# Kernel tuning notes

Hardware: AMD Instinct MI355X
Metric: run time of the kernel (lower is better)

## Reference

```python
import jax, jax.numpy as jnp
import numpy as np

B, L, D = 8, 4096, 768
EPS = 1e-5


def layer_norm(x, g, b):
    mu = jnp.mean(x, axis=-1, keepdims=True)
    var = jnp.mean(jnp.square(x - mu), axis=-1, keepdims=True)
    return (x - mu) * jax.lax.rsqrt(var + EPS) * g + b


def conv1d_same(x_blc, w_oik, b_o):
    # x_blc: [B, L, C] -> torch Conv1d(C, C, 3, padding=1) on [B, C, L]
    x_ncw = jnp.swapaxes(x_blc, 1, 2)
    y = jax.lax.conv_general_dilated(
        x_ncw, w_oik, window_strides=(1,), padding=[(1, 1)],
        dimension_numbers=("NCW", "OIW", "NCW"))
    y = y + b_o[None, :, None]
    return jnp.swapaxes(y, 1, 2)


def simple_ssm(u, a_p, b_p, c_p, d_p):
    # Diagonal SSM: h_t = sigmoid(a)*h_{t-1} + b*u_t ; y_t = c*h_t + d*u_t
    a = jax.nn.sigmoid(a_p)  # [D]

    def step(h, ut):  # h, ut: [B, D]
        h = a * h + b_p * ut
        return h, c_p * h

    h0 = jnp.zeros((u.shape[0], u.shape[2]), u.dtype)
    _, y = jax.lax.scan(step, h0, jnp.swapaxes(u, 0, 1))  # y: [L, B, D]
    return jnp.swapaxes(y, 0, 1) + d_p * u


def setup_inputs() -> dict:
    key = jax.random.key(0)
    ks = jax.random.split(key, 16)
    s_lin = 1.0 / np.sqrt(D)
    s_conv = 1.0 / np.sqrt(3 * D)
    return {
        "x": jax.random.normal(ks[0], (B, L, D), jnp.float32),
        "ln_g": jnp.ones((D,), jnp.float32),
        "ln_b": jnp.zeros((D,), jnp.float32),
        "Wi": jax.random.normal(ks[1], (D, 2 * D), jnp.float32) * s_lin,
        "bi": jnp.zeros((2 * D,), jnp.float32),
        "Wf_conv": jax.random.normal(ks[2], (D, D, 3), jnp.float32) * s_conv,
        "bf_conv": jnp.zeros((D,), jnp.float32),
        "af": jax.random.normal(ks[3], (D,), jnp.float32),
        "bf": jax.random.normal(ks[4], (D,), jnp.float32) * 0.5,
        "cf": jax.random.normal(ks[5], (D,), jnp.float32) * 0.5,
        "df": jax.random.normal(ks[6], (D,), jnp.float32) * 0.5,
        "Wb_conv": jax.random.normal(ks[7], (D, D, 3), jnp.float32) * s_conv,
        "bb_conv": jnp.zeros((D,), jnp.float32),
        "ab": jax.random.normal(ks[8], (D,), jnp.float32),
        "bb": jax.random.normal(ks[9], (D,), jnp.float32) * 0.5,
        "cb": jax.random.normal(ks[10], (D,), jnp.float32) * 0.5,
        "db": jax.random.normal(ks[11], (D,), jnp.float32) * 0.5,
        "Wo": jax.random.normal(ks[12], (D, D), jnp.float32) * s_lin,
        "bo": jnp.zeros((D,), jnp.float32),
    }


def reference(x, ln_g, ln_b, Wi, bi, Wf_conv, bf_conv, af, bf, cf, df,
              Wb_conv, bb_conv, ab, bb, cb, db, Wo, bo):
    residual = x
    xn = layer_norm(x, ln_g, ln_b)
    proj = xn @ Wi + bi                      # [B, L, 2D]
    xg, z = proj[..., :D], proj[..., D:]
    # forward branch
    f = conv1d_same(xg, Wf_conv, bf_conv)
    f = simple_ssm(f, af, bf, cf, df)
    # backward branch (flip along sequence)
    b_in = jnp.flip(xg, axis=1)
    bb_out = conv1d_same(b_in, Wb_conv, bb_conv)
    bb_out = simple_ssm(bb_out, ab, bb, cb, db)
    bb_out = jnp.flip(bb_out, axis=1)
    zg = jax.nn.silu(z)
    y = f * zg + bb_out * zg
    return y @ Wo + bo + residual
```

## Files before the change

kernel.cpp:

```cpp
#include <hip/hip_runtime.h>
#include <cstdint>
#include <cstddef>
#include <math.h>

#define L_SEQ 4096
#define D_DIM 768
#define B_SZ 8
#define M_ROWS (B_SZ * L_SEQ)
#define CHUNK 64

typedef __bf16 bf16x8 __attribute__((ext_vector_type(8)));
typedef float floatx4 __attribute__((ext_vector_type(4)));

__global__ __launch_bounds__(256) void ln_kernel(const float* __restrict__ x,
                                                 const float* __restrict__ g,
                                                 const float* __restrict__ b,
                                                 __bf16* __restrict__ xn) {
  __shared__ float red[256];
  const int tid = threadIdx.x;
  const size_t row = blockIdx.x;
  const float* xr = x + row * D_DIM;
  float v0 = xr[tid];
  float v1 = xr[tid + 256];
  float v2 = xr[tid + 512];
  red[tid] = v0 + v1 + v2;
  __syncthreads();
  for (int off = 128; off > 0; off >>= 1) {
    if (tid < off) red[tid] += red[tid + off];
    __syncthreads();
  }
  float mu = red[0] * (1.0f / D_DIM);
  __syncthreads();
  float d0 = v0 - mu, d1 = v1 - mu, d2 = v2 - mu;
  red[tid] = d0 * d0 + d1 * d1 + d2 * d2;
  __syncthreads();
  for (int off = 128; off > 0; off >>= 1) {
    if (tid < off) red[tid] += red[tid + off];
    __syncthreads();
  }
  float rs = rsqrtf(red[0] * (1.0f / D_DIM) + 1e-5f);
  __bf16* xo = xn + row * D_DIM;
  xo[tid]       = (__bf16)(d0 * rs * g[tid]       + b[tid]);
  xo[tid + 256] = (__bf16)(d1 * rs * g[tid + 256] + b[tid + 256]);
  xo[tid + 512] = (__bf16)(d2 * rs * g[tid + 512] + b[tid + 512]);
}

template<int MODE>
__global__ __launch_bounds__(256) void gemm_kernel(
    const __bf16* __restrict__ A,
    const __bf16* __restrict__ Bt,
    const float* __restrict__ bias,
    const float* __restrict__ resid,
    __bf16* __restrict__ out0,
    __bf16* __restrict__ out1,
    float* __restrict__ outf,
    int K) {
  __shared__ __bf16 As[128 * 40];
  __shared__ __bf16 Bs[128 * 40];
  const int tid  = threadIdx.x;
  const int tileM = blockIdx.x;
  const int tileN = blockIdx.y;
  const int lane = tid & 63;
  const int wv   = tid >> 6;
  const int wm   = wv >> 1;
  const int wn   = wv & 1;
  const int l15  = lane & 15;
  const int quad = lane >> 4;
  const int sr = tid >> 2;
  const int sc = (tid & 3) * 8;

  floatx4 acc[4][4];
#pragma unroll
  for (int i = 0; i < 4; ++i)
#pragma unroll
    for (int j = 0; j < 4; ++j)
#pragma unroll
      for (int r = 0; r < 4; ++r) acc[i][j][r] = 0.0f;

  for (int kt = 0; kt < K; kt += 32) {
    __syncthreads();
#pragma unroll
    for (int p = 0; p < 2; ++p) {
      int r = sr + p * 64;
      bf16x8 av;
      if (MODE == 1 || MODE == 2) {
        int grow = tileM * 128 + r;
        int bidx = grow >> 12;
        int l    = grow & (L_SEQ - 1);
        int kblk = kt / D_DIM;
        int i0   = kt - kblk * D_DIM;
        int lsrc = (MODE == 1) ? (l + kblk - 1) : (L_SEQ - l - kblk);
        if (lsrc >= 0 && lsrc < L_SEQ) {
          av = *(const bf16x8*)(A + ((size_t)(bidx * L_SEQ + lsrc)) * D_DIM + i0 + sc);
        } else {
#pragma unroll
          for (int q = 0; q < 8; ++q) av[q] = (__bf16)0.0f;
        }
      } else {
        size_t grow = (size_t)(tileM * 128 + r);
        av = *(const bf16x8*)(A + grow * (size_t)K + kt + sc);
      }
      *(bf16x8*)(&As[r * 40 + sc]) = av;
      size_t gn = (size_t)(tileN * 128 + r);
      bf16x8 bv = *(const bf16x8*)(Bt + gn * (size_t)K + kt + sc);
      *(bf16x8*)(&Bs[r * 40 + sc]) = bv;
    }
    __syncthreads();

    bf16x8 afr[4], bfr[4];
#pragma unroll
    for (int i = 0; i < 4; ++i)
      afr[i] = *(const bf16x8*)(&As[(wm * 64 + i * 16 + l15) * 40 + quad * 8]);
#pragma unroll
    for (int j = 0; j < 4; ++j)
      bfr[j] = *(const bf16x8*)(&Bs[(wn * 64 + j * 16 + l15) * 40 + quad * 8]);
#pragma unroll
    for (int i = 0; i < 4; ++i)
#pragma unroll
      for (int j = 0; j < 4; ++j)
        acc[i][j] = __builtin_amdgcn_mfma_f32_16x16x32_bf16(afr[i], bfr[j], acc[i][j], 0, 0, 0);
  }

#pragma unroll
  for (int i = 0; i < 4; ++i) {
#pragma unroll
    for (int j = 0; j < 4; ++j) {
#pragma unroll
      for (int r = 0; r < 4; ++r) {
        int row = tileM * 128 + wm * 64 + i * 16 + quad * 4 + r;
        int col = tileN * 128 + wn * 64 + j * 16 + l15;
        float v = acc[i][j][r] + bias[col];
        if (MODE == 0) {
          if (col < D_DIM) {
            out0[(size_t)row * D_DIM + col] = (__bf16)v;
          } else {
            float s = v / (1.0f + expf(-v));
            out1[(size_t)row * D_DIM + (col - D_DIM)] = (__bf16)s;
          }
        } else if (MODE == 3) {
          size_t o = (size_t)row * D_DIM + col;
          outf[o] = v + resid[o];
        } else {
          out0[(size_t)row * D_DIM + col] = (__bf16)v;
        }
      }
    }
  }
}


__global__ __launch_bounds__(256) void scan1_kernel(
    const float* __restrict__ ap0, const float* __restrict__ bp0,
    const float* __restrict__ ap1, const float* __restrict__ bp1,
    const __bf16* __restrict__ u0, const __bf16* __restrict__ u1,
    float* __restrict__ hl) {
  int idx = blockIdx.x * 256 + threadIdx.x;
  int d = idx % D_DIM;
  int rest = idx / D_DIM;
  int chunk = rest & 63;
  int tb = rest >> 6;
  int b = tb & 7;
  int tensor = tb >> 3;
  const float* ap = tensor ? ap1 : ap0;
  const float* bp = tensor ? bp1 : bp0;
  const __bf16* u = (tensor ? u1 : u0) +
      ((size_t)(b * L_SEQ + chunk * CHUNK)) * D_DIM + d;
  float a  = 1.0f / (1.0f + expf(-ap[d]));
  float bb = bp[d];
  float h = 0.0f;
  for (int t = 0; t < CHUNK; ++t) {
    h = a * h + bb * (float)u[(size_t)t * D_DIM];
  }
  hl[(size_t)idx] = h;
}

__global__ __launch_bounds__(256) void scan2_kernel(
    const float* __restrict__ ap0, const float* __restrict__ ap1,
    float* __restrict__ hl) {
  int idx = blockIdx.x * 256 + threadIdx.x;
  int d = idx % D_DIM;
  int tb = idx / D_DIM;
  int tensor = tb >> 3;
  const float* ap = tensor ? ap1 : ap0;
  float a = 1.0f / (1.0f + expf(-ap[d]));
  float aT = a * a;
  aT = aT * aT;
  aT = aT * aT;
  aT = aT * aT;
  aT = aT * aT;
  aT = aT * aT;
  float* base = hl + (size_t)tb * 64 * D_DIM + d;
  float carry = 0.0f;
  for (int c = 0; c < 64; ++c) {
    float* p = base + (size_t)c * D_DIM;
    float tmp = *p;
    *p = carry;
    carry = aT * carry + tmp;
  }
}

__global__ __launch_bounds__(256) void scan3_kernel(
    const float* __restrict__ ap0, const float* __restrict__ bp0,
    const float* __restrict__ cp0, const float* __restrict__ dp0,
    const float* __restrict__ ap1, const float* __restrict__ bp1,
    const float* __restrict__ cp1, const float* __restrict__ dp1,
    __bf16* __restrict__ u0, __bf16* __restrict__ u1,
    const float* __restrict__ hl) {
  int idx = blockIdx.x * 256 + threadIdx.x;
  int d = idx % D_DIM;
  int rest = idx / D_DIM;
  int chunk = rest & 63;
  int tb = rest >> 6;
  int b = tb & 7;
  int tensor = tb >> 3;
  const float* ap = tensor ? ap1 : ap0;
  const float* bp = tensor ? bp1 : bp0;
  const float* cp = tensor ? cp1 : cp0;
  const float* dp = tensor ? dp1 : dp0;
  __bf16* u = (tensor ? u1 : u0) +
      ((size_t)(b * L_SEQ + chunk * CHUNK)) * D_DIM + d;
  float a  = 1.0f / (1.0f + expf(-ap[d]));
  float bb = bp[d];
  float cc = cp[d];
  float dd = dp[d];
  float h = hl[(size_t)idx];
  for (int t = 0; t < CHUNK; ++t) {
    float uv = (float)u[(size_t)t * D_DIM];
    h = a * h + bb * uv;
    u[(size_t)t * D_DIM] = (__bf16)(cc * h + dd * uv);
  }
}

__global__ __launch_bounds__(256) void gate_kernel(const __bf16* __restrict__ f,
                                                   const __bf16* __restrict__ bbuf,
                                                   const __bf16* __restrict__ zg,
                                                   __bf16* __restrict__ y) {
  size_t idx = (size_t)blockIdx.x * 256 + threadIdx.x;
  int d = (int)(idx % D_DIM);
  size_t rl = idx / D_DIM;
  int l = (int)(rl & (L_SEQ - 1));
  size_t b = rl >> 12;
  size_t src = ((b << 12) + (size_t)(L_SEQ - 1 - l)) * D_DIM + d;
  float v = ((float)f[idx] + (float)bbuf[src]) * (float)zg[idx];
  y[idx] = (__bf16)v;
}

__global__ __launch_bounds__(256) void tr_kernel(const float* __restrict__ in,
                                                 __bf16* __restrict__ out,
                                                 int Kdim, int Ndim) {
  int idx = blockIdx.x * 256 + threadIdx.x;
  if (idx >= Kdim * Ndim) return;
  int n = idx / Kdim;
  int k = idx - n * Kdim;
  out[idx] = (__bf16)in[(size_t)k * Ndim + n];
}

__global__ __launch_bounds__(256) void trconv_kernel(const float* __restrict__ in,
                                                     __bf16* __restrict__ out) {
  int idx = blockIdx.x * 256 + threadIdx.x;
  if (idx >= D_DIM * 2304) return;
  int o = idx / 2304;
  int rem = idx - o * 2304;
  int k = rem / D_DIM;
  int i = rem - k * D_DIM;
  out[idx] = (__bf16)in[(size_t)o * 2304 + i * 3 + k];
}

extern "C" void kernel_launch(void* const* d_in, const int* in_sizes, int n_in,
                              void* d_out, int out_size, void* d_ws, size_t ws_size,
                              hipStream_t stream) {
  const float* x    = (const float*)d_in[0];
  const float* ln_g = (const float*)d_in[1];
  const float* ln_b = (const float*)d_in[2];
  const float* Wi   = (const float*)d_in[3];
  const float* bi   = (const float*)d_in[4];
  const float* Wf   = (const float*)d_in[5];
  const float* bfc  = (const float*)d_in[6];
  const float* af   = (const float*)d_in[7];
  const float* bfp  = (const float*)d_in[8];
  const float* cfp  = (const float*)d_in[9];
  const float* dfp  = (const float*)d_in[10];
  const float* Wb   = (const float*)d_in[11];
  const float* bbc  = (const float*)d_in[12];
  const float* ab   = (const float*)d_in[13];
  const float* bbp  = (const float*)d_in[14];
  const float* cbp  = (const float*)d_in[15];
  const float* dbp  = (const float*)d_in[16];
  const float* Wo   = (const float*)d_in[17];
  const float* bo   = (const float*)d_in[18];
  float* out = (float*)d_out;

  char* ws = (char*)d_ws;
  const size_t BLD = (size_t)B_SZ * L_SEQ * D_DIM;
  __bf16* ws0 = (__bf16*)(ws);
  __bf16* ws1 = (__bf16*)(ws + BLD * 2);
  __bf16* ws2 = (__bf16*)(ws + BLD * 4);
  __bf16* ws3 = (__bf16*)(ws + BLD * 6);
  __bf16* wit = (__bf16*)(ws + BLD * 8);
  __bf16* wft = wit + (size_t)1536 * 768;
  __bf16* wbt = wft + (size_t)768 * 2304;
  __bf16* wot = wbt + (size_t)768 * 2304;
  float* hl = (float*)(ws + BLD * 2);
  const size_t needed = BLD * 8 +
      ((size_t)1536 * 768 + 2 * (size_t)768 * 2304 + (size_t)768 * 768) * 2;
  if (ws_size < needed) return;

  tr_kernel<<<(768 * 1536 + 255) / 256, 256, 0, stream>>>(Wi, wit, 768, 1536);
  trconv_kernel<<<(768 * 2304 + 255) / 256, 256, 0, stream>>>(Wf, wft);
  trconv_kernel<<<(768 * 2304 + 255) / 256, 256, 0, stream>>>(Wb, wbt);
  tr_kernel<<<(768 * 768 + 255) / 256, 256, 0, stream>>>(Wo, wot, 768, 768);

  ln_kernel<<<M_ROWS, 256, 0, stream>>>(x, ln_g, ln_b, ws0);

  gemm_kernel<0><<<dim3(M_ROWS / 128, 1536 / 128), 256, 0, stream>>>(
      ws0, wit, bi, nullptr, ws1, ws2, nullptr, 768);

  gemm_kernel<1><<<dim3(M_ROWS / 128, 768 / 128), 256, 0, stream>>>(
      ws1, wft, bfc, nullptr, ws0, nullptr, nullptr, 2304);
  gemm_kernel<2><<<dim3(M_ROWS / 128, 768 / 128), 256, 0, stream>>>(
      ws1, wbt, bbc, nullptr, ws3, nullptr, nullptr, 2304);

  {
    const int n1 = 2 * B_SZ * 64 * D_DIM;
    scan1_kernel<<<n1 / 256, 256, 0, stream>>>(af, bfp, ab, bbp, ws0, ws3, hl);
    const int n2 = 2 * B_SZ * D_DIM;
    scan2_kernel<<<n2 / 256, 256, 0, stream>>>(af, ab, hl);
    scan3_kernel<<<n1 / 256, 256, 0, stream>>>(af, bfp, cfp, dfp,
                                               ab, bbp, cbp, dbp,
                                               ws0, ws3, hl);
  }

  gate_kernel<<<(unsigned)(BLD / 256), 256, 0, stream>>>(ws0, ws3, ws2, ws1);

  gemm_kernel<3><<<dim3(M_ROWS / 128, 768 / 128), 256, 0, stream>>>(
      ws1, wot, bo, x, nullptr, nullptr, out, 768);
}
```

Baseline: 901.7 us.

## Use direct global-to-LDS loads in GEMM and swap grid axes for reuse

The GEMM tile loads now use global_load_lds (buffer-to-LDS DMA), so data no longer passes through registers. Conv boundary rows point at a small zeroed buffer instead of taking a branch. The LDS row stride drops from 40 to 32 because the DMA writes contiguously, which may bring back LDS bank conflicts on fragment reads. The grid is also transposed so N-tiles vary fastest, letting neighbouring blocks share the same A rows in cache, and the k-block/offset bookkeeping becomes incremental instead of a division.

Result: faster. 880.5 us (-2.3%).

```diff
diff --git a/kernel.cpp b/kernel.cpp
--- a/kernel.cpp
+++ b/kernel.cpp
@@ -11,6 +11,9 @@
 
 typedef __bf16 bf16x8 __attribute__((ext_vector_type(8)));
 typedef float floatx4 __attribute__((ext_vector_type(4)));
+
+#define GLP(p)  ((__attribute__((address_space(1))) const void*)(const void*)(p))
+#define LDSP(p) ((__attribute__((address_space(3))) void*)(void*)(p))
 
 __global__ __launch_bounds__(256) void ln_kernel(const float* __restrict__ x,
                                                  const float* __restrict__ g,
@@ -54,20 +57,45 @@
     __bf16* __restrict__ out0,
     __bf16* __restrict__ out1,
     float* __restrict__ outf,
+    const __bf16* __restrict__ zbuf,
     int K) {
-  __shared__ __bf16 As[128 * 40];
-  __shared__ __bf16 Bs[128 * 40];
-  const int tid  = threadIdx.x;
-  const int tileM = blockIdx.x;
-  const int tileN = blockIdx.y;
+  __shared__ __bf16 As[128 * 32];
+  __shared__ __bf16 Bs[128 * 32];
+  const int tid   = threadIdx.x;
+  const int tileN = blockIdx.x;
+  const int tileM = blockIdx.y;
   const int lane = tid & 63;
-  const int wv   = tid >> 6;
-  const int wm   = wv >> 1;
-  const int wn   = wv & 1;
+  const int w    = tid >> 6;
+  const int wm   = w >> 1;
+  const int wn   = w & 1;
   const int l15  = lane & 15;
   const int quad = lane >> 4;
-  const int sr = tid >> 2;
-  const int sc = (tid & 3) * 8;
+  const int colg = (lane & 3) * 8;
+  const int rsub = lane >> 2;
+
+  const int rowA0 = w * 32 + rsub;
+  const int rowA1 = rowA0 + 16;
+
+  const __bf16* gB0 = Bt + (size_t)(tileN * 128 + rowA0) * K + colg;
+  const __bf16* gB1 = Bt + (size_t)(tileN * 128 + rowA1) * K + colg;
+
+  const __bf16* gA0 = nullptr;
+  const __bf16* gA1 = nullptr;
+  int bl0 = 0, bl1 = 0, l0 = 0, l1 = 0;
+  if (MODE == 1 || MODE == 2) {
+    int gr0 = tileM * 128 + rowA0;
+    int gr1 = tileM * 128 + rowA1;
+    bl0 = gr0 >> 12; l0 = gr0 & (L_SEQ - 1);
+    bl1 = gr1 >> 12; l1 = gr1 & (L_SEQ - 1);
+  } else {
+    gA0 = A + (size_t)(tileM * 128 + rowA0) * K + colg;
+    gA1 = A + (size_t)(tileM * 128 + rowA1) * K + colg;
+  }
+
+  __bf16* ldsA0 = &As[(w * 32) * 32];
+  __bf16* ldsA1 = &As[(w * 32 + 16) * 32];
+  __bf16* ldsB0 = &Bs[(w * 32) * 32];
+  __bf16* ldsB1 = &Bs[(w * 32 + 16) * 32];
 
   floatx4 acc[4][4];
 #pragma unroll
@@ -77,48 +105,43 @@
 #pragma unroll
       for (int r = 0; r < 4; ++r) acc[i][j][r] = 0.0f;
 
+  int kblk = 0, i0 = 0;
   for (int kt = 0; kt < K; kt += 32) {
     __syncthreads();
-#pragma unroll
-    for (int p = 0; p < 2; ++p) {
-      int r = sr + p * 64;
-      bf16x8 av;
-      if (MODE == 1 || MODE == 2) {
-        int grow = tileM * 128 + r;
-        int bidx = grow >> 12;
-        int l    = grow & (L_SEQ - 1);
-        int kblk = kt / D_DIM;
-        int i0   = kt - kblk * D_DIM;
-        int lsrc = (MODE == 1) ? (l + kblk - 1) : (L_SEQ - l - kblk);
-        if (lsrc >= 0 && lsrc < L_SEQ) {
-          av = *(const bf16x8*)(A + ((size_t)(bidx * L_SEQ + lsrc)) * D_DIM + i0 + sc);
-        } else {
-#pragma unroll
-          for (int q = 0; q < 8; ++q) av[q] = (__bf16)0.0f;
-        }
-      } else {
-        size_t grow = (size_t)(tileM * 128 + r);
-        av = *(const bf16x8*)(A + grow * (size_t)K + kt + sc);
-      }
-      *(bf16x8*)(&As[r * 40 + sc]) = av;
-      size_t gn = (size_t)(tileN * 128 + r);
-      bf16x8 bv = *(const bf16x8*)(Bt + gn * (size_t)K + kt + sc);
-      *(bf16x8*)(&Bs[r * 40 + sc]) = bv;
+    const __bf16* pa0;
+    const __bf16* pa1;
+    if (MODE == 1 || MODE == 2) {
+      int ls0 = (MODE == 1) ? (l0 + kblk - 1) : (L_SEQ - l0 - kblk);
+      int ls1 = (MODE == 1) ? (l1 + kblk - 1) : (L_SEQ - l1 - kblk);
+      pa0 = (ls0 >= 0 && ls0 < L_SEQ)
+          ? A + ((size_t)(bl0 << 12) + (size_t)ls0) * D_DIM + i0 + colg : zbuf;
+      pa1 = (ls1 >= 0 && ls1 < L_SEQ)
+          ? A + ((size_t)(bl1 << 12) + (size_t)ls1) * D_DIM + i0 + colg : zbuf;
+    } else {
+      pa0 = gA0 + kt;
+      pa1 = gA1 + kt;
     }
+    __builtin_amdgcn_global_load_lds(GLP(pa0), LDSP(ldsA0), 16, 0, 0);
+    __builtin_amdgcn_global_load_lds(GLP(pa1), LDSP(ldsA1), 16, 0, 0);
+    __builtin_amdgcn_global_load_lds(GLP(gB0 + kt), LDSP(ldsB0), 16, 0, 0);
+    __builtin_amdgcn_global_load_lds(GLP(gB1 + kt), LDSP(ldsB1), 16, 0, 0);
     __syncthreads();
 
     bf16x8 afr[4], bfr[4];
 #pragma unroll
     for (int i = 0; i < 4; ++i)
-      afr[i] = *(const bf16x8*)(&As[(wm * 64 + i * 16 + l15) * 40 + quad * 8]);
+      afr[i] = *(const bf16x8*)(&As[(wm * 64 + i * 16 + l15) * 32 + quad * 8]);
 #pragma unroll
     for (int j = 0; j < 4; ++j)
-      bfr[j] = *(const bf16x8*)(&Bs[(wn * 64 + j * 16 + l15) * 40 + quad * 8]);
+      bfr[j] = *(const bf16x8*)(&Bs[(wn * 64 + j * 16 + l15) * 32 + quad * 8]);
 #pragma unroll
     for (int i = 0; i < 4; ++i)
 #pragma unroll
       for (int j = 0; j < 4; ++j)
         acc[i][j] = __builtin_amdgcn_mfma_f32_16x16x32_bf16(afr[i], bfr[j], acc[i][j], 0, 0, 0);
+
+    i0 += 32;
+    if (i0 == D_DIM) { i0 = 0; ++kblk; }
   }
 
 #pragma unroll
@@ -148,7 +171,6 @@
   }
 }
 
-
 __global__ __launch_bounds__(256) void scan1_kernel(
     const float* __restrict__ ap0, const float* __restrict__ bp0,
     const float* __restrict__ ap1, const float* __restrict__ bp1,
@@ -183,12 +205,8 @@
   int tensor = tb >> 3;
   const float* ap = tensor ? ap1 : ap0;
   float a = 1.0f / (1.0f + expf(-ap[d]));
-  float aT = a * a;
-  aT = aT * aT;
-  aT = aT * aT;
-  aT = aT * aT;
-  aT = aT * aT;
-  aT = aT * aT;
+  float aT = a * a;  aT = aT * aT;  aT = aT * aT;
+  aT = aT * aT;      aT = aT * aT;  aT = aT * aT;
   float* base = hl + (size_t)tb * 64 * D_DIM + d;
   float carry = 0.0f;
   for (int c = 0; c < 64; ++c) {
@@ -265,6 +283,8 @@
   int i = rem - k * D_DIM;
   out[idx] = (__bf16)in[(size_t)o * 2304 + i * 3 + k];
 }
+
+__global__ void zero_kernel(__bf16* z) { z[threadIdx.x] = (__bf16)0.0f; }
 
 extern "C" void kernel_launch(void* const* d_in, const int* in_sizes, int n_in,
                               void* d_out, int out_size, void* d_ws, size_t ws_size,
@@ -300,11 +320,13 @@
   __bf16* wft = wit + (size_t)1536 * 768;
   __bf16* wbt = wft + (size_t)768 * 2304;
   __bf16* wot = wbt + (size_t)768 * 2304;
+  __bf16* zbuf = wot + (size_t)768 * 768;
   float* hl = (float*)(ws + BLD * 2);
   const size_t needed = BLD * 8 +
-      ((size_t)1536 * 768 + 2 * (size_t)768 * 2304 + (size_t)768 * 768) * 2;
+      ((size_t)1536 * 768 + 2 * (size_t)768 * 2304 + (size_t)768 * 768) * 2 + 256;
   if (ws_size < needed) return;
 
+  zero_kernel<<<1, 128, 0, stream>>>(zbuf);
   tr_kernel<<<(768 * 1536 + 255) / 256, 256, 0, stream>>>(Wi, wit, 768, 1536);
   trconv_kernel<<<(768 * 2304 + 255) / 256, 256, 0, stream>>>(Wf, wft);
   trconv_kernel<<<(768 * 2304 + 255) / 256, 256, 0, stream>>>(Wb, wbt);
@@ -312,13 +334,13 @@
 
   ln_kernel<<<M_ROWS, 256, 0, stream>>>(x, ln_g, ln_b, ws0);
 
-  gemm_kernel<0><<<dim3(M_ROWS / 128, 1536 / 128), 256, 0, stream>>>(
-      ws0, wit, bi, nullptr, ws1, ws2, nullptr, 768);
-
-  gemm_kernel<1><<<dim3(M_ROWS / 128, 768 / 128), 256, 0, stream>>>(
-      ws1, wft, bfc, nullptr, ws0, nullptr, nullptr, 2304);
-  gemm_kernel<2><<<dim3(M_ROWS / 128, 768 / 128), 256, 0, stream>>>(
-      ws1, wbt, bbc, nullptr, ws3, nullptr, nullptr, 2304);
+  gemm_kernel<0><<<dim3(1536 / 128, M_ROWS / 128), 256, 0, stream>>>(
+      ws0, wit, bi, nullptr, ws1, ws2, nullptr, zbuf, 768);
+
+  gemm_kernel<1><<<dim3(768 / 128, M_ROWS / 128), 256, 0, stream>>>(
+      ws1, wft, bfc, nullptr, ws0, nullptr, nullptr, zbuf, 2304);
+  gemm_kernel<2><<<dim3(768 / 128, M_ROWS / 128), 256, 0, stream>>>(
+      ws1, wbt, bbc, nullptr, ws3, nullptr, nullptr, zbuf, 2304);
 
   {
     const int n1 = 2 * B_SZ * 64 * D_DIM;
@@ -332,6 +354,6 @@
 
   gate_kernel<<<(unsigned)(BLD / 256), 256, 0, stream>>>(ws0, ws3, ws2, ws1);
 
-  gemm_kernel<3><<<dim3(M_ROWS / 128, 768 / 128), 256, 0, stream>>>(
-      ws1, wot, bo, x, nullptr, nullptr, out, 768);
-}
+  gemm_kernel<3><<<dim3(768 / 128, M_ROWS / 128), 256, 0, stream>>>(
+      ws1, wot, bo, x, nullptr, nullptr, out, zbuf, 768);
+}
```
